# Performance work log

Hardware: AMD Instinct MI355X
Metric: run time of the kernel (lower is better)

The kernel has to match this reference:

```python
import jax, jax.numpy as jnp
import numpy as np

IMG = 2048
STRIDES = [8, 16, 32, 64, 128]
A = 9                       # num_cell_anchors
CLASS_NUM = 16              # num_classes - 1
TOPK = 1000                 # config.test_layer_topk
MAX_DELTA = float(np.log(1000.0 / 16.0))

_LEVEL_N = [(IMG // s) * (IMG // s) * A for s in STRIDES]


def setup_inputs() -> dict:
    key = jax.random.key(0)
    inp = {}
    for l, n in enumerate(_LEVEL_N):
        key, k1, k2, k3, k4 = jax.random.split(key, 5)
        cxcy = jax.random.uniform(k1, (n, 2), minval=0.0, maxval=float(IMG))
        wh = jax.random.uniform(k2, (n, 2), minval=8.0, maxval=128.0)
        inp[f"anchors{l}"] = jnp.concatenate([cxcy - 0.5 * wh, cxcy + 0.5 * wh], axis=1)
        # logits biased negative like a trained RetinaNet cls head (prior_prob init)
        inp[f"cls{l}"] = jax.random.normal(k3, (1, n, CLASS_NUM), dtype=jnp.float32) - 4.0
        inp[f"reg{l}"] = jax.random.normal(k4, (1, n, 8), dtype=jnp.float32) * 0.1
    return inp


def bbox_transform_inv(rois, deltas):
    # standard box decode (restore_bbox with unnormalize=False)
    w = rois[:, 2] - rois[:, 0]
    h = rois[:, 3] - rois[:, 1]
    cx = rois[:, 0] + 0.5 * w
    cy = rois[:, 1] + 0.5 * h
    pcx = cx + deltas[:, 0] * w
    pcy = cy + deltas[:, 1] * h
    pw = w * jnp.exp(jnp.minimum(deltas[:, 2], MAX_DELTA))
    ph = h * jnp.exp(jnp.minimum(deltas[:, 3], MAX_DELTA))
    return jnp.stack([pcx - 0.5 * pw, pcy - 0.5 * ph,
                      pcx + 0.5 * pw, pcy + 0.5 * ph], axis=1)


def _per_layer(anchors, pred_cls, pred_reg):
    a = anchors.reshape(-1, 4)
    c = pred_cls[0].reshape(-1, CLASS_NUM)
    r = pred_reg[0].reshape(-1, 8)[:, :4]
    if a.shape[0] > TOPK:
        ruler = jnp.max(c, axis=1)                  # max score over classes
        _, inds = jax.lax.top_k(ruler, TOPK)        # irregular topk + gather
        a = jnp.take(a, inds, axis=0)
        c = jnp.take(c, inds, axis=0)
        r = jnp.take(r, inds, axis=0)
    return a, jax.nn.sigmoid(c), r


def reference(anchors0, cls0, reg0, anchors1, cls1, reg1, anchors2, cls2, reg2,
              anchors3, cls3, reg3, anchors4, cls4, reg4):
    levels = [(anchors0, cls0, reg0), (anchors1, cls1, reg1),
              (anchors2, cls2, reg2), (anchors3, cls3, reg3),
              (anchors4, cls4, reg4)]
    kept = [_per_layer(a, c, r) for a, c, r in levels]
    keep_anchors = jnp.concatenate([k[0] for k in kept], axis=0)   # [K,4]
    keep_cls = jnp.concatenate([k[1] for k in kept], axis=0)       # [K,C]
    keep_reg = jnp.concatenate([k[2] for k in kept], axis=0)       # [K,4]
    K = keep_cls.shape[0]
    tag = jnp.tile(jnp.arange(CLASS_NUM, dtype=keep_cls.dtype) + 1.0, (K,)).reshape(-1, 1)
    pred_scores = keep_cls.reshape(-1, 1)                          # [K*C,1]
    pred_bbox = bbox_transform_inv(keep_anchors, keep_reg)         # [K,4]
    pred_bbox = jnp.tile(pred_bbox, (1, CLASS_NUM)).reshape(-1, 4) # [K*C,4]
    return jnp.concatenate([pred_bbox, pred_scores, tag], axis=1)  # [K*C,6]
```

## Files before the change

### kernel.cpp

```cpp
#include <hip/hip_runtime.h>
#include <math.h>

#define NLEV 5
#define TOPKK 1000
#define NCLS 16
#define NPART 16
#define PART_CAP 256
#define CAND_TOT 2048
#define NTOT 785664u
#define HISTSZ (NLEV * 256)

__device__ __forceinline__ int find_level(unsigned i, unsigned& loc) {
    if (i < 589824u) { loc = i;            return 0; }
    if (i < 737280u) { loc = i - 589824u;  return 1; }
    if (i < 774144u) { loc = i - 737280u;  return 2; }
    if (i < 783360u) { loc = i - 774144u;  return 3; }
    loc = i - 783360u; return 4;
}

struct Ptrs {
    const float* anc[NLEV];
    const float* cls[NLEV];
    const float* reg[NLEV];
};

__device__ __forceinline__ unsigned f2key(float f) {
    unsigned u = __float_as_uint(f);
    return (u & 0x80000000u) ? ~u : (u | 0x80000000u);
}

__device__ __forceinline__ float max4(float4 v) {
    return fmaxf(fmaxf(v.x, v.y), fmaxf(v.z, v.w));
}

__device__ void level_select(const unsigned* histbase, int l, int shift,
                             unsigned rem_in, unsigned pf_acc,
                             unsigned* s, unsigned* aux) {
    int t = threadIdx.x, r = 255 - t;
    unsigned c = 0;
    #pragma unroll
    for (int pp = 0; pp < NPART; pp++) c += histbase[pp * HISTSZ + l * 256 + t];
    s[r] = c;
    __syncthreads();
    for (int d = 1; d < 256; d <<= 1) {
        unsigned v = (r >= d) ? s[r - d] : 0u;
        __syncthreads();
        s[r] += v;
        __syncthreads();
    }
    unsigned incl = s[r], above = incl - c;
    if (above < rem_in && rem_in <= incl) {
        aux[0] = pf_acc | (((unsigned)t) << shift);
        aux[1] = rem_in - above;
    }
    __syncthreads();
}

__global__ __launch_bounds__(256) void k_keys_hist(Ptrs p, unsigned* keys,
                                                   unsigned* hist) {
    __shared__ unsigned lh[256];
    lh[threadIdx.x] = 0u;
    __syncthreads();
    unsigned i = blockIdx.x * 256u + threadIdx.x;
    unsigned loc; int l = find_level(i, loc);
    const float4* c = (const float4*)(p.cls[l]) + (size_t)loc * 4;
    float4 a = c[0], b = c[1], d = c[2], e = c[3];
    float m = max4(a);
    m = fmaxf(m, max4(b));
    m = fmaxf(m, max4(d));
    m = fmaxf(m, max4(e));
    unsigned k = f2key(m);
    keys[i] = k;
    atomicAdd(&lh[k >> 24], 1u);
    __syncthreads();
    unsigned part = blockIdx.x & (NPART - 1);
    if (lh[threadIdx.x])
        atomicAdd(&hist[part * HISTSZ + l * 256 + threadIdx.x], lh[threadIdx.x]);
}

__global__ __launch_bounds__(256) void k_hist2(const unsigned* keys,
                                               const unsigned* histA,
                                               unsigned* histB) {
    __shared__ unsigned s[256];
    __shared__ unsigned lh[256];
    __shared__ unsigned aux[2];
    unsigned i0 = blockIdx.x * 256u;
    unsigned loc0; int l = find_level(i0, loc0);
    level_select(histA, l, 24, TOPKK, 0u, s, aux);
    unsigned pf = aux[0];
    lh[threadIdx.x] = 0u;
    __syncthreads();
    unsigned k = keys[i0 + threadIdx.x];
    if ((k & 0xFF000000u) == pf)
        atomicAdd(&lh[(k >> 16) & 0xFFu], 1u);
    __syncthreads();
    unsigned part = blockIdx.x & (NPART - 1);
    if (lh[threadIdx.x])
        atomicAdd(&histB[part * HISTSZ + l * 256 + threadIdx.x], lh[threadIdx.x]);
}

__global__ __launch_bounds__(256) void k_compact(const unsigned* keys,
                                                 const unsigned* histA,
                                                 const unsigned* histB,
                                                 unsigned* cnt,
                                                 unsigned long long* cand) {
    __shared__ unsigned s[256];
    __shared__ unsigned aux[2];
    unsigned i0 = blockIdx.x * 256u;
    unsigned loc0; int l = find_level(i0, loc0);
    level_select(histA, l, 24, TOPKK, 0u, s, aux);
    unsigned pf1 = aux[0], rem1 = aux[1];
    __syncthreads();
    level_select(histB, l, 16, rem1, pf1, s, aux);
    unsigned thresh = aux[0];
    unsigned k = keys[i0 + threadIdx.x];
    if (k >= thresh) {
        unsigned loc = loc0 + threadIdx.x;
        unsigned part = blockIdx.x & (NPART - 1);
        unsigned slot = atomicAdd(&cnt[l * NPART + part], 1u);
        if (slot < PART_CAP)
            cand[((size_t)(l * NPART + part)) * PART_CAP + slot] =
                ((unsigned long long)k << 32) | (unsigned)(~loc);
    }
}

__global__ __launch_bounds__(256) void k_rank_emit(Ptrs p, const unsigned* cnt,
                                                   const unsigned long long* cand,
                                                   float* out) {
    const float MAXD = 4.135166556742356f;
    int l = blockIdx.x >> 3;
    unsigned sl = blockIdx.x & 7;
    int t = threadIdx.x;
    __shared__ unsigned long long lbuf[CAND_TOT];
    __shared__ unsigned aux[33];

    if (t < NPART) {
        unsigned cc = cnt[l * NPART + t];
        aux[t] = (cc > PART_CAP) ? PART_CAP : cc;
    }
    __syncthreads();
    if (t == 0) {
        unsigned o = 0;
        for (int pp = 0; pp < NPART; pp++) { aux[16 + pp] = o; o += aux[pp]; }
        aux[32] = (o > CAND_TOT) ? CAND_TOT : o;
    }
    __syncthreads();
    unsigned n = aux[32];
    for (int pp = 0; pp < NPART; pp++) {
        unsigned cc = aux[pp], o = aux[16 + pp];
        for (unsigned e = t; e < cc; e += 256) {
            unsigned dst = o + e;
            if (dst < CAND_TOT)
                lbuf[dst] = cand[((size_t)(l * NPART + pp)) * PART_CAP + e];
        }
    }
    __syncthreads();

    unsigned j = sl * 256u + t;
    if (j >= n) return;
    unsigned long long my = lbuf[j];
    unsigned rank = 0;
    #pragma unroll 8
    for (unsigned q = 0; q < n; q++) rank += (lbuf[q] > my) ? 1u : 0u;
    if (rank >= TOPKK) return;

    unsigned idx = ~((unsigned)(my & 0xFFFFFFFFull));
    float4 an = ((const float4*)p.anc[l])[idx];
    float4 dd = ((const float4*)p.reg[l])[(size_t)idx * 2];
    float w = an.z - an.x, h = an.w - an.y;
    float cx = an.x + 0.5f * w, cy = an.y + 0.5f * h;
    float pcx = cx + dd.x * w, pcy = cy + dd.y * h;
    float pw = w * expf(fminf(dd.z, MAXD));
    float ph = h * expf(fminf(dd.w, MAXD));
    float bx = pcx - 0.5f * pw, by = pcy - 0.5f * ph;
    float bz = pcx + 0.5f * pw, bw = pcy + 0.5f * ph;

    const float4* cp = (const float4*)(p.cls[l]) + (size_t)idx * 4;
    float sg[16];
    #pragma unroll
    for (int g = 0; g < 4; g++) {
        float4 v = cp[g];
        sg[4 * g + 0] = 1.0f / (1.0f + expf(-v.x));
        sg[4 * g + 1] = 1.0f / (1.0f + expf(-v.y));
        sg[4 * g + 2] = 1.0f / (1.0f + expf(-v.z));
        sg[4 * g + 3] = 1.0f / (1.0f + expf(-v.w));
    }
    float4* q = (float4*)(out + (size_t)(l * TOPKK + rank) * (NCLS * 6));
    #pragma unroll
    for (int g = 0; g < 8; g++) {
        float ta = (float)(2 * g + 1), tb = (float)(2 * g + 2);
        q[3 * g + 0] = make_float4(bx, by, bz, bw);
        q[3 * g + 1] = make_float4(sg[2 * g], ta, bx, by);
        q[3 * g + 2] = make_float4(bz, bw, sg[2 * g + 1], tb);
    }
}

extern "C" void kernel_launch(void* const* d_in, const int* in_sizes, int n_in,
                              void* d_out, int out_size, void* d_ws, size_t ws_size,
                              hipStream_t stream) {
    Ptrs p;
    for (int l = 0; l < NLEV; l++) {
        p.anc[l] = (const float*)d_in[3 * l + 0];
        p.cls[l] = (const float*)d_in[3 * l + 1];
        p.reg[l] = (const float*)d_in[3 * l + 2];
    }
    char* w = (char*)d_ws;
    unsigned* keys  = (unsigned*)w;
    unsigned* histA = (unsigned*)(w + 3142656);
    unsigned* histB = (unsigned*)(w + 3224576);
    unsigned* cnt   = (unsigned*)(w + 3306496);
    unsigned long long* cand = (unsigned long long*)(w + 3306816);

    float* out = (float*)d_out;
    int nb = NTOT / 256;

    (void)hipMemsetAsync(histA, 0, 164160, stream);
    k_keys_hist<<<nb, 256, 0, stream>>>(p, keys, histA);
    k_hist2<<<nb, 256, 0, stream>>>(keys, histA, histB);
    k_compact<<<nb, 256, 0, stream>>>(keys, histA, histB, cnt, cand);
    k_rank_emit<<<NLEV * 8, 256, 0, stream>>>(p, cnt, cand, out);
}
```

Baseline: 188.0 us.

## Fuse radix-select pipeline into one persistent kernel with grid barriers

Replaces the four separate kernel launches with a single persistent kernel whose block count comes from occupancy, and separates the phases with a hierarchical software grid barrier. Per-level threshold selection now runs once per level and is published through global memory, instead of being recomputed redundantly in every block of the hist2 and compact passes. This is meant to remove launch gaps and the duplicated 16-partition histogram reductions and scans. The cost is spin-wait barrier latency and reliance on all blocks being co-resident. Each block also loops over several chunks, which reduces parallel slack.

```diff
diff --git a/kernel.cpp b/kernel.cpp
--- a/kernel.cpp
+++ b/kernel.cpp
@@ -7,7 +7,7 @@
 #define NPART 16
 #define PART_CAP 256
 #define CAND_TOT 2048
-#define NTOT 785664u
+#define NCHUNK 3069u
 #define HISTSZ (NLEV * 256)
 
 __device__ __forceinline__ int find_level(unsigned i, unsigned& loc) {
@@ -33,13 +33,37 @@
     return fmaxf(fmaxf(v.x, v.y), fmaxf(v.z, v.w));
 }
 
-__device__ void level_select(const unsigned* histbase, int l, int shift,
-                             unsigned rem_in, unsigned pf_acc,
-                             unsigned* s, unsigned* aux) {
+__device__ __forceinline__ void gridbar(unsigned* bar, unsigned nb) {
+    __syncthreads();
+    if (threadIdx.x == 0) {
+        __threadfence();
+        unsigned* gen = bar + 160;
+        unsigned g = __hip_atomic_load(gen, __ATOMIC_ACQUIRE, __HIP_MEMORY_SCOPE_AGENT);
+        unsigned grp = blockIdx.x & 7u;
+        unsigned gsz = (nb + 7u - grp) / 8u;
+        unsigned a = __hip_atomic_fetch_add(bar + grp * 16u, 1u,
+                        __ATOMIC_ACQ_REL, __HIP_MEMORY_SCOPE_AGENT);
+        if (a == gsz - 1u) {
+            __hip_atomic_store(bar + grp * 16u, 0u,
+                               __ATOMIC_RELAXED, __HIP_MEMORY_SCOPE_AGENT);
+            unsigned m = __hip_atomic_fetch_add(bar + 144u, 1u,
+                            __ATOMIC_ACQ_REL, __HIP_MEMORY_SCOPE_AGENT);
+            if (m == 7u) {
+                __hip_atomic_store(bar + 144u, 0u,
+                                   __ATOMIC_RELAXED, __HIP_MEMORY_SCOPE_AGENT);
+                __hip_atomic_fetch_add(gen, 1u,
+                                       __ATOMIC_ACQ_REL, __HIP_MEMORY_SCOPE_AGENT);
+            }
+        }
+        while (__hip_atomic_load(gen, __ATOMIC_ACQUIRE, __HIP_MEMORY_SCOPE_AGENT) == g)
+            __builtin_amdgcn_s_sleep(2);
+        __threadfence();
+    }
+    __syncthreads();
+}
+
+__device__ void suffix_select(unsigned c, unsigned rem, unsigned* s, unsigned* aux) {
     int t = threadIdx.x, r = 255 - t;
-    unsigned c = 0;
-    #pragma unroll
-    for (int pp = 0; pp < NPART; pp++) c += histbase[pp * HISTSZ + l * 256 + t];
     s[r] = c;
     __syncthreads();
     for (int d = 1; d < 256; d <<= 1) {
@@ -49,90 +73,99 @@
         __syncthreads();
     }
     unsigned incl = s[r], above = incl - c;
-    if (above < rem_in && rem_in <= incl) {
-        aux[0] = pf_acc | (((unsigned)t) << shift);
-        aux[1] = rem_in - above;
-    }
-    __syncthreads();
-}
-
-__global__ __launch_bounds__(256) void k_keys_hist(Ptrs p, unsigned* keys,
-                                                   unsigned* hist) {
-    __shared__ unsigned lh[256];
-    lh[threadIdx.x] = 0u;
-    __syncthreads();
-    unsigned i = blockIdx.x * 256u + threadIdx.x;
-    unsigned loc; int l = find_level(i, loc);
-    const float4* c = (const float4*)(p.cls[l]) + (size_t)loc * 4;
-    float4 a = c[0], b = c[1], d = c[2], e = c[3];
-    float m = max4(a);
-    m = fmaxf(m, max4(b));
-    m = fmaxf(m, max4(d));
-    m = fmaxf(m, max4(e));
-    unsigned k = f2key(m);
-    keys[i] = k;
-    atomicAdd(&lh[k >> 24], 1u);
-    __syncthreads();
-    unsigned part = blockIdx.x & (NPART - 1);
-    if (lh[threadIdx.x])
-        atomicAdd(&hist[part * HISTSZ + l * 256 + threadIdx.x], lh[threadIdx.x]);
-}
-
-__global__ __launch_bounds__(256) void k_hist2(const unsigned* keys,
-                                               const unsigned* histA,
-                                               unsigned* histB) {
-    __shared__ unsigned s[256];
-    __shared__ unsigned lh[256];
-    __shared__ unsigned aux[2];
-    unsigned i0 = blockIdx.x * 256u;
-    unsigned loc0; int l = find_level(i0, loc0);
-    level_select(histA, l, 24, TOPKK, 0u, s, aux);
-    unsigned pf = aux[0];
-    lh[threadIdx.x] = 0u;
-    __syncthreads();
-    unsigned k = keys[i0 + threadIdx.x];
-    if ((k & 0xFF000000u) == pf)
-        atomicAdd(&lh[(k >> 16) & 0xFFu], 1u);
-    __syncthreads();
-    unsigned part = blockIdx.x & (NPART - 1);
-    if (lh[threadIdx.x])
-        atomicAdd(&histB[part * HISTSZ + l * 256 + threadIdx.x], lh[threadIdx.x]);
-}
-
-__global__ __launch_bounds__(256) void k_compact(const unsigned* keys,
-                                                 const unsigned* histA,
-                                                 const unsigned* histB,
-                                                 unsigned* cnt,
-                                                 unsigned long long* cand) {
-    __shared__ unsigned s[256];
-    __shared__ unsigned aux[2];
-    unsigned i0 = blockIdx.x * 256u;
-    unsigned loc0; int l = find_level(i0, loc0);
-    level_select(histA, l, 24, TOPKK, 0u, s, aux);
-    unsigned pf1 = aux[0], rem1 = aux[1];
-    __syncthreads();
-    level_select(histB, l, 16, rem1, pf1, s, aux);
-    unsigned thresh = aux[0];
-    unsigned k = keys[i0 + threadIdx.x];
-    if (k >= thresh) {
-        unsigned loc = loc0 + threadIdx.x;
-        unsigned part = blockIdx.x & (NPART - 1);
-        unsigned slot = atomicAdd(&cnt[l * NPART + part], 1u);
-        if (slot < PART_CAP)
-            cand[((size_t)(l * NPART + part)) * PART_CAP + slot] =
-                ((unsigned long long)k << 32) | (unsigned)(~loc);
-    }
-}
-
-__global__ __launch_bounds__(256) void k_rank_emit(Ptrs p, const unsigned* cnt,
-                                                   const unsigned long long* cand,
-                                                   float* out) {
+    if (above < rem && rem <= incl) {
+        aux[0] = (unsigned)t;
+        aux[1] = rem - above;
+    }
+    __syncthreads();
+}
+
+__global__ __launch_bounds__(256, 4) void k_fused(Ptrs p, unsigned* keys,
+        unsigned* histA, unsigned* histB, unsigned* cnt, unsigned* bar,
+        unsigned* selg, unsigned* thresh_g, unsigned long long* cand,
+        float* out, unsigned nb) {
+    __shared__ union ShU {
+        unsigned long long lbuf[CAND_TOT];
+        unsigned s[256];
+    } sh;
+    __shared__ unsigned aux[33];
+    __shared__ unsigned lsh[NLEV];
+
+    const unsigned b = blockIdx.x;
+    const int t = threadIdx.x;
+
+    for (unsigned c = b; c < NCHUNK; c += nb) {
+        unsigned loc; int l = find_level(c * 256u + (unsigned)t, loc);
+        const float4* cp = (const float4*)(p.cls[l]) + (size_t)loc * 4;
+        float4 v0 = cp[0], v1 = cp[1], v2 = cp[2], v3 = cp[3];
+        float m = fmaxf(fmaxf(max4(v0), max4(v1)), fmaxf(max4(v2), max4(v3)));
+        unsigned k = f2key(m);
+        keys[c * 256u + (unsigned)t] = k;
+        sh.s[t] = 0u;
+        __syncthreads();
+        atomicAdd(&sh.s[k >> 24], 1u);
+        __syncthreads();
+        unsigned part = c & (NPART - 1u);
+        if (sh.s[t])
+            atomicAdd(&histA[part * HISTSZ + (unsigned)l * 256u + (unsigned)t], sh.s[t]);
+        __syncthreads();
+    }
+    gridbar(bar, nb);
+
+    if (b < NLEV) {
+        unsigned c = 0;
+        #pragma unroll
+        for (int pp = 0; pp < NPART; pp++) c += histA[pp * HISTSZ + b * 256u + (unsigned)t];
+        suffix_select(c, TOPKK, sh.s, aux);
+        if (t == 0) { selg[2u * b] = aux[0]; selg[2u * b + 1u] = aux[1]; }
+    }
+    gridbar(bar, nb);
+
+    if (t < NLEV) lsh[t] = selg[2u * (unsigned)t];
+    __syncthreads();
+    for (unsigned c = b; c < NCHUNK; c += nb) {
+        unsigned loc; int l = find_level(c * 256u + (unsigned)t, loc);
+        unsigned k = keys[c * 256u + (unsigned)t];
+        sh.s[t] = 0u;
+        __syncthreads();
+        if ((k >> 24) == lsh[l]) atomicAdd(&sh.s[(k >> 16) & 0xFFu], 1u);
+        __syncthreads();
+        unsigned part = c & (NPART - 1u);
+        if (sh.s[t])
+            atomicAdd(&histB[part * HISTSZ + (unsigned)l * 256u + (unsigned)t], sh.s[t]);
+        __syncthreads();
+    }
+    gridbar(bar, nb);
+
+    if (b < NLEV) {
+        unsigned pf = selg[2u * b], rem1 = selg[2u * b + 1u];
+        unsigned c = 0;
+        #pragma unroll
+        for (int pp = 0; pp < NPART; pp++) c += histB[pp * HISTSZ + b * 256u + (unsigned)t];
+        suffix_select(c, rem1, sh.s, aux);
+        if (t == 0) thresh_g[b] = (pf << 24) | (aux[0] << 16);
+    }
+    gridbar(bar, nb);
+
+    if (t < NLEV) lsh[t] = thresh_g[t];
+    __syncthreads();
+    for (unsigned c = b; c < NCHUNK; c += nb) {
+        unsigned loc; int l = find_level(c * 256u + (unsigned)t, loc);
+        unsigned k = keys[c * 256u + (unsigned)t];
+        if (k >= lsh[l]) {
+            unsigned part = c & (NPART - 1u);
+            unsigned slot = atomicAdd(&cnt[l * NPART + part], 1u);
+            if (slot < PART_CAP)
+                cand[((size_t)(l * NPART + part)) * PART_CAP + slot] =
+                    ((unsigned long long)k << 32) | (unsigned)(~loc);
+        }
+    }
+    gridbar(bar, nb);
+
+    if (b >= (unsigned)(NLEV * 8)) return;
     const float MAXD = 4.135166556742356f;
-    int l = blockIdx.x >> 3;
-    unsigned sl = blockIdx.x & 7;
-    int t = threadIdx.x;
-    __shared__ unsigned long long lbuf[CAND_TOT];
-    __shared__ unsigned aux[33];
+    int l = (int)(b >> 3);
+    unsigned sl = b & 7u;
 
     if (t < NPART) {
         unsigned cc = cnt[l * NPART + t];
@@ -148,20 +181,20 @@
     unsigned n = aux[32];
     for (int pp = 0; pp < NPART; pp++) {
         unsigned cc = aux[pp], o = aux[16 + pp];
-        for (unsigned e = t; e < cc; e += 256) {
+        for (unsigned e = (unsigned)t; e < cc; e += 256u) {
             unsigned dst = o + e;
             if (dst < CAND_TOT)
-                lbuf[dst] = cand[((size_t)(l * NPART + pp)) * PART_CAP + e];
+                sh.lbuf[dst] = cand[((size_t)(l * NPART + pp)) * PART_CAP + e];
         }
     }
     __syncthreads();
 
-    unsigned j = sl * 256u + t;
+    unsigned j = sl * 256u + (unsigned)t;
     if (j >= n) return;
-    unsigned long long my = lbuf[j];
+    unsigned long long my = sh.lbuf[j];
     unsigned rank = 0;
     #pragma unroll 8
-    for (unsigned q = 0; q < n; q++) rank += (lbuf[q] > my) ? 1u : 0u;
+    for (unsigned q = 0; q < n; q++) rank += (sh.lbuf[q] > my) ? 1u : 0u;
     if (rank >= TOPKK) return;
 
     unsigned idx = ~((unsigned)(my & 0xFFFFFFFFull));
@@ -198,25 +231,43 @@
 extern "C" void kernel_launch(void* const* d_in, const int* in_sizes, int n_in,
                               void* d_out, int out_size, void* d_ws, size_t ws_size,
                               hipStream_t stream) {
+    (void)in_sizes; (void)n_in; (void)out_size; (void)ws_size;
     Ptrs p;
     for (int l = 0; l < NLEV; l++) {
         p.anc[l] = (const float*)d_in[3 * l + 0];
         p.cls[l] = (const float*)d_in[3 * l + 1];
         p.reg[l] = (const float*)d_in[3 * l + 2];
     }
+
+    static unsigned s_nb = 0;
+    if (s_nb == 0) {
+        int bpcu = 0;
+        if (hipOccupancyMaxActiveBlocksPerMultiprocessor(
+                &bpcu, (const void*)k_fused, 256, 0) != hipSuccess || bpcu < 1)
+            bpcu = 1;
+        int dev = 0, ncu = 0;
+        (void)hipGetDevice(&dev);
+        if (hipDeviceGetAttribute(&ncu, hipDeviceAttributeMultiprocessorCount,
+                                  dev) != hipSuccess || ncu < 1)
+            ncu = 256;
+        unsigned long long nb = (unsigned long long)bpcu * (unsigned long long)ncu;
+        if (nb > 1024ull) nb = 1024ull;
+        if (nb < 64ull) nb = 64ull;
+        s_nb = (unsigned)nb;
+    }
+
     char* w = (char*)d_ws;
-    unsigned* keys  = (unsigned*)w;
-    unsigned* histA = (unsigned*)(w + 3142656);
-    unsigned* histB = (unsigned*)(w + 3224576);
-    unsigned* cnt   = (unsigned*)(w + 3306496);
-    unsigned long long* cand = (unsigned long long*)(w + 3306816);
-
+    unsigned* histA = (unsigned*)w;
+    unsigned* histB = (unsigned*)(w + 81920);
+    unsigned* cnt   = (unsigned*)(w + 163840);
+    unsigned* bar   = (unsigned*)(w + 164160);
+    unsigned* selg  = (unsigned*)(w + 165184);
+    unsigned* thr   = (unsigned*)(w + 165248);
+    unsigned* keys  = (unsigned*)(w + 165312);
+    unsigned long long* cand = (unsigned long long*)(w + 3307968);
     float* out = (float*)d_out;
-    int nb = NTOT / 256;
-
-    (void)hipMemsetAsync(histA, 0, 164160, stream);
-    k_keys_hist<<<nb, 256, 0, stream>>>(p, keys, histA);
-    k_hist2<<<nb, 256, 0, stream>>>(keys, histA, histB);
-    k_compact<<<nb, 256, 0, stream>>>(keys, histA, histB, cnt, cand);
-    k_rank_emit<<<NLEV * 8, 256, 0, stream>>>(p, cnt, cand, out);
-}
+
+    (void)hipMemsetAsync(w, 0, 165184, stream);
+    k_fused<<<dim3(s_nb), dim3(256), 0, stream>>>(p, keys, histA, histB, cnt,
+                                                  bar, selg, thr, cand, out, s_nb);
+}
```

Result: slower. 687.4 us (+265.6%).

## Replace two-pass radix histogram with single 16-bit global histogram and select kernel

Applied to the files above, without the earlier changes.

Builds one 16-bit-prefix histogram per level (4 partitions, swizzled bins) with direct global atomics in the key pass, so the separate second histogram pass over all keys is no longer needed. A small per-level select kernel finds the threshold once, and compaction just reads it instead of every block redoing the prefix scans. In exchange there is a 5 MB memset, heavy global atomic contention on hot bins of the negatively biased score distribution, and a 5-block select kernel that serially reads 64K bins per level.

```diff
diff --git a/kernel.cpp b/kernel.cpp
--- a/kernel.cpp
+++ b/kernel.cpp
@@ -5,10 +5,12 @@
 #define TOPKK 1000
 #define NCLS 16
 #define NPART 16
+#define HPART 4
 #define PART_CAP 256
 #define CAND_TOT 2048
 #define NTOT 785664u
-#define HISTSZ (NLEV * 256)
+#define HIST16_LEV 65536u
+#define HIST16_PART (NLEV * HIST16_LEV)
 
 __device__ __forceinline__ int find_level(unsigned i, unsigned& loc) {
     if (i < 589824u) { loc = i;            return 0; }
@@ -33,13 +35,8 @@
     return fmaxf(fmaxf(v.x, v.y), fmaxf(v.z, v.w));
 }
 
-__device__ void level_select(const unsigned* histbase, int l, int shift,
-                             unsigned rem_in, unsigned pf_acc,
-                             unsigned* s, unsigned* aux) {
+__device__ void suffix_select(unsigned c, unsigned rem, unsigned* s, unsigned* aux) {
     int t = threadIdx.x, r = 255 - t;
-    unsigned c = 0;
-    #pragma unroll
-    for (int pp = 0; pp < NPART; pp++) c += histbase[pp * HISTSZ + l * 256 + t];
     s[r] = c;
     __syncthreads();
     for (int d = 1; d < 256; d <<= 1) {
@@ -49,70 +46,65 @@
         __syncthreads();
     }
     unsigned incl = s[r], above = incl - c;
-    if (above < rem_in && rem_in <= incl) {
-        aux[0] = pf_acc | (((unsigned)t) << shift);
-        aux[1] = rem_in - above;
-    }
-    __syncthreads();
-}
-
-__global__ __launch_bounds__(256) void k_keys_hist(Ptrs p, unsigned* keys,
-                                                   unsigned* hist) {
-    __shared__ unsigned lh[256];
-    lh[threadIdx.x] = 0u;
-    __syncthreads();
+    if (above < rem && rem <= incl) {
+        aux[0] = (unsigned)t;
+        aux[1] = rem - above;
+    }
+    __syncthreads();
+}
+
+__global__ __launch_bounds__(256) void k_keys_hist16(Ptrs p, unsigned* keys,
+                                                     unsigned* hist16) {
     unsigned i = blockIdx.x * 256u + threadIdx.x;
     unsigned loc; int l = find_level(i, loc);
     const float4* c = (const float4*)(p.cls[l]) + (size_t)loc * 4;
     float4 a = c[0], b = c[1], d = c[2], e = c[3];
-    float m = max4(a);
-    m = fmaxf(m, max4(b));
-    m = fmaxf(m, max4(d));
-    m = fmaxf(m, max4(e));
+    float m = fmaxf(fmaxf(max4(a), max4(b)), fmaxf(max4(d), max4(e)));
     unsigned k = f2key(m);
     keys[i] = k;
-    atomicAdd(&lh[k >> 24], 1u);
-    __syncthreads();
-    unsigned part = blockIdx.x & (NPART - 1);
-    if (lh[threadIdx.x])
-        atomicAdd(&hist[part * HISTSZ + l * 256 + threadIdx.x], lh[threadIdx.x]);
-}
-
-__global__ __launch_bounds__(256) void k_hist2(const unsigned* keys,
-                                               const unsigned* histA,
-                                               unsigned* histB) {
+    unsigned bin = k >> 16;
+    unsigned swz = ((bin & 0xFFu) << 8) | (bin >> 8);
+    unsigned part = threadIdx.x >> 6;
+    atomicAdd(&hist16[part * HIST16_PART + (unsigned)l * HIST16_LEV + swz], 1u);
+}
+
+__global__ __launch_bounds__(256) void k_select(const unsigned* hist16,
+                                                unsigned* thresh_g) {
     __shared__ unsigned s[256];
-    __shared__ unsigned lh[256];
     __shared__ unsigned aux[2];
+    int l = blockIdx.x, t = threadIdx.x;
+    const unsigned base = (unsigned)l * HIST16_LEV;
+
+    unsigned tot = 0;
+    #pragma unroll 8
+    for (int j = 0; j < 256; j++) {
+        unsigned idx = (unsigned)(j * 256 + t);
+        #pragma unroll
+        for (int pp = 0; pp < HPART; pp++)
+            tot += hist16[pp * HIST16_PART + base + idx];
+    }
+    suffix_select(tot, TOPKK, s, aux);
+    unsigned C = aux[0], rem = aux[1];
+    __syncthreads();
+
+    unsigned fc = 0;
+    {
+        unsigned idx = (unsigned)t * 256u + C;
+        #pragma unroll
+        for (int pp = 0; pp < HPART; pp++)
+            fc += hist16[pp * HIST16_PART + base + idx];
+    }
+    suffix_select(fc, rem, s, aux);
+    if (t == 0) thresh_g[l] = (C << 24) | (aux[0] << 16);
+}
+
+__global__ __launch_bounds__(256) void k_compact(const unsigned* keys,
+                                                 const unsigned* thresh_g,
+                                                 unsigned* cnt,
+                                                 unsigned long long* cand) {
     unsigned i0 = blockIdx.x * 256u;
     unsigned loc0; int l = find_level(i0, loc0);
-    level_select(histA, l, 24, TOPKK, 0u, s, aux);
-    unsigned pf = aux[0];
-    lh[threadIdx.x] = 0u;
-    __syncthreads();
-    unsigned k = keys[i0 + threadIdx.x];
-    if ((k & 0xFF000000u) == pf)
-        atomicAdd(&lh[(k >> 16) & 0xFFu], 1u);
-    __syncthreads();
-    unsigned part = blockIdx.x & (NPART - 1);
-    if (lh[threadIdx.x])
-        atomicAdd(&histB[part * HISTSZ + l * 256 + threadIdx.x], lh[threadIdx.x]);
-}
-
-__global__ __launch_bounds__(256) void k_compact(const unsigned* keys,
-                                                 const unsigned* histA,
-                                                 const unsigned* histB,
-                                                 unsigned* cnt,
-                                                 unsigned long long* cand) {
-    __shared__ unsigned s[256];
-    __shared__ unsigned aux[2];
-    unsigned i0 = blockIdx.x * 256u;
-    unsigned loc0; int l = find_level(i0, loc0);
-    level_select(histA, l, 24, TOPKK, 0u, s, aux);
-    unsigned pf1 = aux[0], rem1 = aux[1];
-    __syncthreads();
-    level_select(histB, l, 16, rem1, pf1, s, aux);
-    unsigned thresh = aux[0];
+    unsigned thresh = thresh_g[l];
     unsigned k = keys[i0 + threadIdx.x];
     if (k >= thresh) {
         unsigned loc = loc0 + threadIdx.x;
@@ -198,6 +190,7 @@
 extern "C" void kernel_launch(void* const* d_in, const int* in_sizes, int n_in,
                               void* d_out, int out_size, void* d_ws, size_t ws_size,
                               hipStream_t stream) {
+    (void)in_sizes; (void)n_in; (void)out_size; (void)ws_size;
     Ptrs p;
     for (int l = 0; l < NLEV; l++) {
         p.anc[l] = (const float*)d_in[3 * l + 0];
@@ -205,18 +198,17 @@
         p.reg[l] = (const float*)d_in[3 * l + 2];
     }
     char* w = (char*)d_ws;
-    unsigned* keys  = (unsigned*)w;
-    unsigned* histA = (unsigned*)(w + 3142656);
-    unsigned* histB = (unsigned*)(w + 3224576);
-    unsigned* cnt   = (unsigned*)(w + 3306496);
-    unsigned long long* cand = (unsigned long long*)(w + 3306816);
-
+    unsigned* hist16 = (unsigned*)w;
+    unsigned* cnt    = (unsigned*)(w + 5242880);
+    unsigned* thr    = (unsigned*)(w + 5243200);
+    unsigned* keys   = (unsigned*)(w + 5243264);
+    unsigned long long* cand = (unsigned long long*)(w + 8385920);
     float* out = (float*)d_out;
     int nb = NTOT / 256;
 
-    (void)hipMemsetAsync(histA, 0, 164160, stream);
-    k_keys_hist<<<nb, 256, 0, stream>>>(p, keys, histA);
-    k_hist2<<<nb, 256, 0, stream>>>(keys, histA, histB);
-    k_compact<<<nb, 256, 0, stream>>>(keys, histA, histB, cnt, cand);
+    (void)hipMemsetAsync(w, 0, 5243200, stream);
+    k_keys_hist16<<<nb, 256, 0, stream>>>(p, keys, hist16);
+    k_select<<<NLEV, 256, 0, stream>>>(hist16, thr);
+    k_compact<<<nb, 256, 0, stream>>>(keys, thr, cnt, cand);
     k_rank_emit<<<NLEV * 8, 256, 0, stream>>>(p, cnt, cand, out);
 }
```

New measurement: 225.3 us. 1.2x slower.
